# Kernel optimization log

Measured on AMD Instinct MI355X. Metric: run time of the kernel, lower is better.

Reference implementation:

```python
import jax, jax.numpy as jnp
import numpy as np

L = 4        # num_layers
N = 50000    # nodes
E = 500000   # edges
B = 32       # graphs
H = 64       # hidden_dim
HP = 16      # hidden_dim_pe
P = 8        # pe_dim
BN_EPS = 1e-5


def setup_inputs() -> dict:
    key = jax.random.key(0)
    ks = jax.random.split(key, 22)
    nrm = lambda k, s: jax.random.normal(k, s, dtype=jnp.float32)
    w = lambda k, s: nrm(k, s) * 0.1
    return {
        'x': nrm(ks[0], (N, H)),
        'pe': nrm(ks[1], (N, P)),
        'Lambda': jax.random.uniform(ks[2], (B, P), dtype=jnp.float32),
        'edge_attr': nrm(ks[3], (E, H)),
        'edge_index': jax.random.randint(ks[4], (2, E), 0, N),
        'batch': jnp.sort(jax.random.randint(ks[5], (N,), 0, B)),
        # edge encoder (SPE): eigenvalue MLP + output projection
        'We1': w(ks[6], (L, P, HP * P)), 'be1': jnp.zeros((L, HP * P)),
        'Wee': w(ks[7], (L, HP, H)),     'bee': jnp.zeros((L, H)),
        # GINE mlp: Linear-BN-ReLU-Linear
        'W1': w(ks[8], (L, H, H)), 'b1': jnp.zeros((L, H)),
        'g1': jnp.ones((L, H)),    'beta1': jnp.zeros((L, H)),
        'W2': w(ks[9], (L, H, H)), 'b2': jnp.zeros((L, H)),
        # equivariant PE conv: edge gate + channel Linear
        'Wg': w(ks[10], (L, H, HP)),  'bg': jnp.zeros((L, HP)),
        'Wp': w(ks[11], (L, HP, HP)), 'bp': jnp.zeros((L, HP)),
        # outer BatchNorm per layer
        'gn': jnp.ones((L, H)), 'bnb': jnp.zeros((L, H)),
    }


def _bn(h, gamma, beta):
    mu = h.mean(0)
    var = h.var(0)
    return gamma * (h - mu) * jax.lax.rsqrt(var + BN_EPS) + beta


def reference(x, pe, Lambda, edge_attr, We1, be1, Wee, bee, W1, b1, g1, beta1,
              W2, b2, Wg, bg, Wp, bp, gn, bnb, edge_index, batch):
    src, dst = edge_index[0], edge_index[1]
    bsrc = batch[src]                       # [E] graph id of source node
    z = jnp.tile(pe[:, None, :], (1, HP, 1))  # [N, HP, P]
    for i in range(L):
        # SPE edge encoder: phi(Lambda)-weighted inner product over pe axis
        phi = jax.nn.relu(Lambda @ We1[i] + be1[i]).reshape(B, HP, P)
        eh = jnp.einsum('ehp,ehp->eh', phi[bsrc] * z[src], z[dst])  # [E, HP]
        ea = eh @ Wee[i] + bee[i] + edge_attr                       # [E, H]
        # GINEConv: scatter-add of relu(x_src + edge_attr), eps = 0
        agg = jax.ops.segment_sum(jax.nn.relu(x[src] + ea), dst, num_segments=N)
        h = x + agg
        h = jax.nn.relu(_bn(h @ W1[i] + b1[i], g1[i], beta1[i])) @ W2[i] + b2[i]
        # GINConvEquivariant: gated scatter-add, Linear on channel axis
        gate = jax.nn.relu(ea @ Wg[i] + bg[i])                      # [E, HP]
        msgz = jax.nn.relu(z[src] + gate[:, :, None])               # [E, HP, P]
        z = z + jax.ops.segment_sum(msgz, dst, num_segments=N)
        z = jnp.einsum('nhp,hk->nkp', z, Wp[i]) + bp[i][None, :, None]
        x = _bn(h, gn[i], bnb[i])
        if i != L - 1:
            x = jax.nn.relu(x)
    return x, z
```

## Files before the change

### kernel.cpp

```cpp
#include <hip/hip_runtime.h>

#define NN 50000
#define EE 500000
#define LL 4

typedef unsigned short u16;
typedef unsigned int u32;

__device__ __forceinline__ float bfc(u16 u) { return __uint_as_float(((u32)u) << 16); }
__device__ __forceinline__ u16 f2bf(float f) {
    u32 u = __float_as_uint(f);
    return (u16)((u + 0x7fffu + ((u >> 16) & 1u)) >> 16);
}
__device__ __forceinline__ float lanebc(float v, int l) {
    return __int_as_float(__builtin_amdgcn_readlane(__float_as_int(v), l));
}
__device__ __forceinline__ void unpack2(u32 w, float& lo, float& hi) {
    lo = __uint_as_float(w << 16);
    hi = __uint_as_float(w & 0xffff0000u);
}

__global__ __launch_bounds__(256) void k_init(const float* __restrict__ x, float* __restrict__ Xf,
                                              u16* __restrict__ Xh, int big,
                                              int* __restrict__ deg, int* __restrict__ cursor,
                                              double* __restrict__ statsAll) {
    for (int i = blockIdx.x * 256 + threadIdx.x; i < NN * 64; i += gridDim.x * 256) {
        if (big) Xh[i] = f2bf(x[i]);
        else Xf[i] = x[i];
    }
    for (int i = blockIdx.x * 256 + threadIdx.x; i < NN; i += gridDim.x * 256) {
        deg[i] = 0;
        cursor[i] = 0;
    }
    for (int i = blockIdx.x * 256 + threadIdx.x; i < LL * 256; i += gridDim.x * 256)
        statsAll[i] = 0.0;
}

__global__ __launch_bounds__(128) void k_phi(const float* __restrict__ Lam, const float* __restrict__ We1,
                                             const float* __restrict__ be1, float* __restrict__ phiA) {
    int l = blockIdx.x >> 5, b = blockIdx.x & 31, j = threadIdx.x;
    float acc = be1[l * 128 + j];
    for (int q = 0; q < 8; q++)
        acc = fmaf(Lam[b * 8 + q], We1[l * 1024 + q * 128 + j], acc);
    phiA[l * 4096 + b * 128 + j] = fmaxf(acc, 0.f);
}

__global__ __launch_bounds__(256) void k_small(const float* __restrict__ Wee, const float* __restrict__ Wg,
                                               float* __restrict__ MA) {
    int l = blockIdx.x, t = threadIdx.x;
    int k = t >> 4, h = t & 15;
    float m = 0.f;
    for (int f = 0; f < 64; f++)
        m = fmaf(Wee[l * 1024 + k * 64 + f], Wg[l * 1024 + f * 16 + h], m);
    MA[l * 256 + t] = m;
}

__global__ __launch_bounds__(256) void k_hist(const int* __restrict__ ei, int* __restrict__ deg) {
    int e = blockIdx.x * 256 + threadIdx.x;
    if (e < EE) {
        int d = ei[EE + e];
        if (d >= 0 && d < NN) atomicAdd(&deg[d], 1);
    }
}

__global__ __launch_bounds__(256) void k_scan1(const int* __restrict__ deg, int* __restrict__ rowptr,
                                               int* __restrict__ bsum) {
    __shared__ int tmp[256];
    int t = threadIdx.x, i = blockIdx.x * 256 + t;
    int v = (i < NN) ? deg[i] : 0;
    tmp[t] = v;
    __syncthreads();
    for (int off = 1; off < 256; off <<= 1) {
        int a = (t >= off) ? tmp[t - off] : 0;
        __syncthreads();
        tmp[t] += a;
        __syncthreads();
    }
    if (i < NN) rowptr[i] = tmp[t] - v;
    if (t == 255) bsum[blockIdx.x] = tmp[255];
}

__global__ __launch_bounds__(256) void k_scan2(const int* __restrict__ bsum, int* __restrict__ boff,
                                               int* __restrict__ rowptr, int nb) {
    __shared__ int tmp[256];
    int t = threadIdx.x;
    int v = (t < nb) ? bsum[t] : 0;
    tmp[t] = v;
    __syncthreads();
    for (int off = 1; off < 256; off <<= 1) {
        int a = (t >= off) ? tmp[t - off] : 0;
        __syncthreads();
        tmp[t] += a;
        __syncthreads();
    }
    if (t < nb) boff[t] = tmp[t] - v;
    if (t == 255) rowptr[NN] = tmp[255];
}

__global__ __launch_bounds__(256) void k_scan3(int* __restrict__ rowptr, const int* __restrict__ boff) {
    int i = blockIdx.x * 256 + threadIdx.x;
    if (i < NN) rowptr[i] += boff[blockIdx.x];
}

__global__ __launch_bounds__(256) void k_scatter(const int* __restrict__ ei, const int* __restrict__ batch,
                                                 const int* __restrict__ rowptr, int* __restrict__ cursor,
                                                 u32* __restrict__ sb, int* __restrict__ eeo) {
    int e = blockIdx.x * 256 + threadIdx.x;
    if (e < EE) {
        int s = ei[e], d = ei[EE + e];
        if (s < 0) s = 0; if (s >= NN) s = NN - 1;
        if (d < 0) d = 0; if (d >= NN) d = NN - 1;
        int pos = rowptr[d] + atomicAdd(&cursor[d], 1);
        if (pos >= 0 && pos < EE) {
            sb[pos] = (u32)s | ((u32)(batch[s] & 31) << 16);
            eeo[pos] = e;
        }
    }
}

__global__ __launch_bounds__(256) void k_perm(const float* __restrict__ eat, const int* __restrict__ eeo,
                                              u16* __restrict__ eatp) {
    const float4* e4 = reinterpret_cast<const float4*>(eat);
    ushort4* o4 = reinterpret_cast<ushort4*>(eatp);
    for (long long i = (long long)blockIdx.x * 256 + threadIdx.x; i < (long long)EE * 16;
         i += (long long)gridDim.x * 256) {
        int idx = (int)(i >> 4), cc = (int)(i & 15);
        int e = eeo[idx];
        float4 v = e4[(size_t)e * 16 + cc];
        ushort4 o;
        o.x = f2bf(v.x); o.y = f2bf(v.y); o.z = f2bf(v.z); o.w = f2bf(v.w);
        o4[i] = o;
    }
}

__global__ __launch_bounds__(256) void k_eag_all(const u16* __restrict__ eatp, const float* __restrict__ Wg,
                                                 const float* __restrict__ bee, const float* __restrict__ bg,
                                                 u32* __restrict__ EAGp4) {
    __shared__ float sWg[4096];
    __shared__ float scv[64];
    __shared__ u32 srow[256][33];
    const int t = threadIdx.x;
    for (int i = t; i < 4096; i += 256) sWg[i] = Wg[i];
    __syncthreads();
    if (t < 64) {
        const int l = t >> 4, h = t & 15;
        float c = bg[l * 16 + h];
        for (int j = 0; j < 64; j++) c = fmaf(bee[l * 64 + j], sWg[l * 1024 + j * 16 + h], c);
        scv[t] = c;
    }
    const int base = blockIdx.x * 256;
    const u32* eat32 = (const u32*)eatp;
    for (int i = t; i < 256 * 32; i += 256) {
        int r = i >> 5, c = i & 31;
        int idx = base + r;
        srow[r][c] = (idx < EE) ? eat32[(size_t)idx * 32 + c] : 0u;
    }
    __syncthreads();
    const int idx = base + t;
    if (idx >= EE) return;
#pragma unroll
    for (int l = 0; l < LL; l++) {
        const float* wl = &sWg[l * 1024];
        float acc[16];
#pragma unroll
        for (int h = 0; h < 16; h++) acc[h] = scv[l * 16 + h];
#pragma unroll
        for (int c = 0; c < 32; c++) {
            float a0, a1;
            unpack2(srow[t][c], a0, a1);
            const float* w0 = &wl[(2 * c) * 16];
#pragma unroll
            for (int h = 0; h < 16; h++) acc[h] = fmaf(a0, w0[h], fmaf(a1, w0[16 + h], acc[h]));
        }
        u32 w[8];
#pragma unroll
        for (int h = 0; h < 8; h++) w[h] = (u32)f2bf(acc[h]) | ((u32)f2bf(acc[8 + h]) << 16);
        uint4* op = reinterpret_cast<uint4*>(EAGp4 + (size_t)l * EE * 8 + (size_t)idx * 8);
        op[0] = make_uint4(w[0], w[1], w[2], w[3]);
        op[1] = make_uint4(w[4], w[5], w[6], w[7]);
    }
}

__global__ __launch_bounds__(256) void k_eag2(const u16* __restrict__ eatp, const float* __restrict__ WgL,
                                              const float* __restrict__ beeL, const float* __restrict__ bgL,
                                              u32* __restrict__ EAGp) {
    __shared__ float sWg[1024];
    __shared__ float scv[16];
    __shared__ u32 srow[256][33];
    const int t = threadIdx.x;
    for (int i = t; i < 1024; i += 256) sWg[i] = WgL[i];
    __syncthreads();
    if (t < 16) {
        float c = bgL[t];
        for (int j = 0; j < 64; j++) c = fmaf(beeL[j], sWg[j * 16 + t], c);
        scv[t] = c;
    }
    const int base = blockIdx.x * 256;
    const u32* eat32 = (const u32*)eatp;
    for (int i = t; i < 256 * 32; i += 256) {
        int r = i >> 5, c = i & 31;
        int idx = base + r;
        srow[r][c] = (idx < EE) ? eat32[(size_t)idx * 32 + c] : 0u;
    }
    __syncthreads();
    const int idx = base + t;
    if (idx < EE) {
        float acc[16];
#pragma unroll
        for (int h = 0; h < 16; h++) acc[h] = scv[h];
#pragma unroll
        for (int c = 0; c < 32; c++) {
            float a0, a1;
            unpack2(srow[t][c], a0, a1);
            const float* w0 = &sWg[(2 * c) * 16];
#pragma unroll
            for (int h = 0; h < 16; h++) acc[h] = fmaf(a0, w0[h], fmaf(a1, w0[16 + h], acc[h]));
        }
        u32 w[8];
#pragma unroll
        for (int h = 0; h < 8; h++) w[h] = (u32)f2bf(acc[h]) | ((u32)f2bf(acc[8 + h]) << 16);
        uint4* op = reinterpret_cast<uint4*>(EAGp + (size_t)idx * 8);
        op[0] = make_uint4(w[0], w[1], w[2], w[3]);
        op[1] = make_uint4(w[4], w[5], w[6], w[7]);
    }
}

#define EF(P, kk) do { \
    P##w = (u32)__builtin_amdgcn_readlane((int)svec, (kk)); \
    int s_ = (int)(P##w & 0xffffu); \
    if (INM == 0) { P##z0 = P##z1 = pe[s_ * 8 + pp]; } \
    else { float2 t_ = Z2[s_ * 64 + lane]; P##z0 = t_.x; P##z1 = t_.y; } \
    P##xs = XBN ? fmaxf(0.f, fmaf(bfc(Xh[s_ * 64 + lane]), gmx, gax)) \
                : bfc(Xh[s_ * 64 + lane]); \
    size_t ge_ = (size_t)(c + (kk)); \
    P##ea = bfc(eatp[ge_ * 64 + lane]); \
    unpack2(EAGp[ge_ * 8 + hlo], P##gl, P##gh); \
} while (0)

#define EC(P, MSK) do { \
    int b_ = (int)((P##w >> 16) & 31u); \
    float p0 = sphi[b_ * 128 + lane] * P##z0 * zd0; \
    float p1 = sphi[b_ * 128 + 64 + lane] * P##z1 * zd1; \
    p0 += __shfl_xor(p0, 1); p1 += __shfl_xor(p1, 1); \
    p0 += __shfl_xor(p0, 2); p1 += __shfl_xor(p1, 2); \
    p0 += __shfl_xor(p0, 4); p1 += __shfl_xor(p1, 4); \
    float eaA = 0.f, eaB = 0.f, gA = P##gl, gB = 0.f, hA = P##gh, hB = 0.f; \
    _Pragma("unroll") \
    for (int k_ = 0; k_ < 8; k_++) { float e_ = lanebc(p0, k_ << 3); \
        eaA = fmaf(e_, wee[k_], eaA); gA = fmaf(e_, mlo[k_], gA); hA = fmaf(e_, mhi[k_], hA); } \
    _Pragma("unroll") \
    for (int k_ = 0; k_ < 8; k_++) { float e_ = lanebc(p1, k_ << 3); \
        eaB = fmaf(e_, wee[8 + k_], eaB); gB = fmaf(e_, mlo[8 + k_], gB); hB = fmaf(e_, mhi[8 + k_], hB); } \
    float ea_ = beev + P##ea + eaA + eaB; \
    accx = fmaf(MSK, fmaxf(0.f, P##xs + ea_), accx); \
    az0  = fmaf(MSK, fmaxf(0.f, P##z0 + fmaxf(gA + gB, 0.f)), az0); \
    az1  = fmaf(MSK, fmaxf(0.f, P##z1 + fmaxf(hA + hB, 0.f)), az1); \
} while (0)

template <int INM, int FIN, int XBN>
__global__ __launch_bounds__(256) void k_edge2(const float2* __restrict__ Z2,
                                               const float* __restrict__ pe,
                                               const u16* __restrict__ Xh,
                                               const u16* __restrict__ eatp, const u32* __restrict__ EAGp,
                                               const int* __restrict__ rowptr, const u32* __restrict__ sb,
                                               const float* __restrict__ phiL, const float* __restrict__ WeeL,
                                               const float* __restrict__ beeL, const float* __restrict__ ML,
                                               const float* __restrict__ WpL, const float* __restrict__ bpL,
                                               float* __restrict__ Hf, float2* __restrict__ Z2O,
                                               float* __restrict__ outz,
                                               const float* __restrict__ gnP, const float* __restrict__ bnbP,
                                               const double* __restrict__ s2P, const double* __restrict__ q2P) {
    __shared__ float sphi[4096];
    __shared__ float sWp[256];
    __shared__ float sbp[16];
    for (int t = threadIdx.x; t < 4096; t += 256) sphi[t] = phiL[t];
    if (threadIdx.x < 256) sWp[threadIdx.x] = WpL[threadIdx.x];
    if (threadIdx.x < 16) sbp[threadIdx.x] = bpL[threadIdx.x];
    const int lane = threadIdx.x & 63;
    const int wid = threadIdx.x >> 6;
    const int hlo = lane >> 3;
    const int pp = lane & 7;
    float wee[16], mlo[16], mhi[16];
#pragma unroll
    for (int k = 0; k < 16; k++) {
        wee[k] = WeeL[k * 64 + lane];
        mlo[k] = ML[k * 16 + hlo];
        mhi[k] = ML[k * 16 + 8 + hlo];
    }
    const float beev = beeL[lane];
    float gmx = 1.f, gax = 0.f;
    if (XBN) {
        const double mu = s2P[lane] * (1.0 / NN);
        const double var = q2P[lane] * (1.0 / NN) - mu * mu;
        const float inv = rsqrtf(fmaxf((float)var, 0.f) + 1e-5f);
        gmx = gnP[lane] * inv;
        gax = bnbP[lane] - (float)mu * gmx;
    }
    __syncthreads();
    for (int n = blockIdx.x * 4 + wid; n < NN; n += gridDim.x * 4) {
        float zd0, zd1;
        if (INM == 0) { zd0 = zd1 = pe[n * 8 + pp]; }
        else { float2 t = Z2[n * 64 + lane]; zd0 = t.x; zd1 = t.y; }
        float accx = XBN ? fmaxf(0.f, fmaf(bfc(Xh[n * 64 + lane]), gmx, gax))
                         : bfc(Xh[n * 64 + lane]);
        float az0 = zd0, az1 = zd1;
        int i0 = rowptr[n], i1 = rowptr[n + 1];
        if (i0 < 0) i0 = 0;
        if (i1 > EE) i1 = EE;
        for (int c = i0; c < i1; c += 64) {
            const int ce = (c + 64 < i1) ? c + 64 : i1;
            const int m = ce - c;
            const int mL = m - 1;
            int ci = c + lane; if (ci > i1 - 1) ci = i1 - 1;
            const u32 svec = sb[ci];
            u32 Aw, Bw, Nw, Mw;
            float Az0, Az1, Axs, Aea, Agl, Agh;
            float Bz0, Bz1, Bxs, Bea, Bgl, Bgh;
            float Nz0, Nz1, Nxs, Nea, Ngl, Ngh;
            float Mz0, Mz1, Mxs, Mea, Mgl, Mgh;
            EF(A, 0);
            EF(B, (1 > mL ? mL : 1));
            for (int k = 0; k < m; k += 2) {
                const int n0 = (k + 2 > mL) ? mL : k + 2;
                const int n1 = (k + 3 > mL) ? mL : k + 3;
                EF(N, n0);
                EF(M, n1);
                EC(A, 1.f);
                EC(B, (k + 1 <= mL) ? 1.f : 0.f);
                Aw = Nw; Az0 = Nz0; Az1 = Nz1; Axs = Nxs; Aea = Nea; Agl = Ngl; Agh = Ngh;
                Bw = Mw; Bz0 = Mz0; Bz1 = Mz1; Bxs = Mxs; Bea = Mea; Bgl = Mgl; Bgh = Mgh;
            }
        }
        Hf[n * 64 + lane] = accx;
        float r0 = sbp[hlo], r1 = sbp[8 + hlo];
#pragma unroll
        for (int h = 0; h < 8; h++) {
            const float v = __shfl(az0, (h << 3) + pp);
            r0 = fmaf(v, sWp[h * 16 + hlo], r0);
            r1 = fmaf(v, sWp[h * 16 + 8 + hlo], r1);
        }
#pragma unroll
        for (int h = 0; h < 8; h++) {
            const float v = __shfl(az1, (h << 3) + pp);
            r0 = fmaf(v, sWp[(8 + h) * 16 + hlo], r0);
            r1 = fmaf(v, sWp[(8 + h) * 16 + 8 + hlo], r1);
        }
        if (FIN) {
            outz[n * 128 + lane] = r0;
            outz[n * 128 + 64 + lane] = r1;
        } else {
            Z2O[n * 64 + lane] = make_float2(r0, r1);
        }
    }
}

template <int INM>
__global__ __launch_bounds__(256) void k_edge_s(const float* __restrict__ Zf,
                                                const float* __restrict__ pe,
                                                const float* __restrict__ Xf, const float* __restrict__ eat,
                                                const int* __restrict__ rowptr, const u32* __restrict__ sb,
                                                const int* __restrict__ eeo,
                                                const float* __restrict__ phiL, const float* __restrict__ WeeL,
                                                const float* __restrict__ beeL,
                                                const float* __restrict__ WgL, const float* __restrict__ bgL,
                                                const float* __restrict__ WpL, const float* __restrict__ bpL,
                                                float* __restrict__ Hf, float* __restrict__ ZfO,
                                                double* __restrict__ stats) {
    __shared__ float sphi[32 * 128];
    __shared__ float sWp[256];
    __shared__ float sbp[16];
    if (blockIdx.x == 0) stats[threadIdx.x] = 0.0;
    for (int t = threadIdx.x; t < 4096; t += 256) sphi[t] = phiL[t];
    if (threadIdx.x < 256) sWp[threadIdx.x] = WpL[threadIdx.x];
    if (threadIdx.x < 16) sbp[threadIdx.x] = bpL[threadIdx.x];
    const int lane = threadIdx.x & 63;
    const int wid = threadIdx.x >> 6;
    const int hlo = lane >> 3;
    const int pp = lane & 7;
    const int h16 = lane & 15;
    const int g16 = lane & 48;
    float wee[16], wgr[16];
#pragma unroll
    for (int k = 0; k < 16; k++) {
        wee[k] = WeeL[k * 64 + lane];
        wgr[k] = WgL[(g16 + k) * 16 + h16];
    }
    const float beev = beeL[lane];
    const float bgr = bgL[h16];
    __syncthreads();
    for (int n = blockIdx.x * 4 + wid; n < NN; n += gridDim.x * 4) {
        float zd0, zd1;
        if (INM == 0) { zd0 = zd1 = pe[n * 8 + pp]; }
        else { zd0 = Zf[n * 128 + lane]; zd1 = Zf[n * 128 + 64 + lane]; }
        float accx = Xf[n * 64 + lane];
        float az0 = zd0, az1 = zd1;
        int i0 = rowptr[n], i1 = rowptr[n + 1];
        if (i0 < 0) i0 = 0;
        if (i1 > EE) i1 = EE;
        for (int idx = i0; idx < i1; ++idx) {
            const u32 w = sb[idx];
            const int s = w & 0xffff;
            const int b = (w >> 16) & 31;
            int e = eeo[idx];
            e = (e < 0) ? 0 : ((e >= EE) ? EE - 1 : e);
            float zs0, zs1;
            if (INM == 0) { zs0 = zs1 = pe[s * 8 + pp]; }
            else { zs0 = Zf[s * 128 + lane]; zs1 = Zf[s * 128 + 64 + lane]; }
            float p0 = sphi[b * 128 + lane] * zs0 * zd0;
            float p1 = sphi[b * 128 + 64 + lane] * zs1 * zd1;
            p0 += __shfl_xor(p0, 1); p1 += __shfl_xor(p1, 1);
            p0 += __shfl_xor(p0, 2); p1 += __shfl_xor(p1, 2);
            p0 += __shfl_xor(p0, 4); p1 += __shfl_xor(p1, 4);
            float ea = beev + eat[(size_t)e * 64 + lane];
#pragma unroll
            for (int k = 0; k < 8; k++) ea = fmaf(lanebc(p0, k << 3), wee[k], ea);
#pragma unroll
            for (int k = 0; k < 8; k++) ea = fmaf(lanebc(p1, k << 3), wee[8 + k], ea);
            float gp = 0.f;
#pragma unroll
            for (int i = 0; i < 16; i++) gp = fmaf(__shfl(ea, g16 + i), wgr[i], gp);
            gp += __shfl_xor(gp, 16);
            gp += __shfl_xor(gp, 32);
            const float gv = fmaxf(gp + bgr, 0.f);
            const float glo = __shfl(gv, hlo);
            const float ghi = __shfl(gv, 8 + hlo);
            const float xs = Xf[s * 64 + lane];
            accx += fmaxf(0.f, xs + ea);
            az0 += fmaxf(0.f, zs0 + glo);
            az1 += fmaxf(0.f, zs1 + ghi);
        }
        Hf[n * 64 + lane] = accx;
        float r0 = sbp[hlo], r1 = sbp[8 + hlo];
#pragma unroll
        for (int h = 0; h < 8; h++) {
            const float v = __shfl(az0, (h << 3) + pp);
            r0 = fmaf(v, sWp[h * 16 + hlo], r0);
            r1 = fmaf(v, sWp[h * 16 + 8 + hlo], r1);
        }
#pragma unroll
        for (int h = 0; h < 8; h++) {
            const float v = __shfl(az1, (h << 3) + pp);
            r0 = fmaf(v, sWp[(8 + h) * 16 + hlo], r0);
            r1 = fmaf(v, sWp[(8 + h) * 16 + 8 + hlo], r1);
        }
        ZfO[n * 128 + lane] = r0;
        ZfO[n * 128 + 64 + lane] = r1;
    }
}

__global__ __launch_bounds__(256) void k_gemm1(float* Buf, const float* __restrict__ WL,
                                               const float* __restrict__ bL,
                                               double* __restrict__ sum, double* __restrict__ sq) {
    __shared__ float sW[4096];
    __shared__ double red[512];
    for (int t = threadIdx.x; t < 4096; t += 256) sW[t] = WL[t];
    const int lane = threadIdx.x & 63, wid = threadIdx.x >> 6;
    const float bv = bL[lane];
    __syncthreads();
    double s = 0.0, q = 0.0;
    for (int n = blockIdx.x * 4 + wid; n < NN; n += gridDim.x * 4) {
        const float h = Buf[n * 64 + lane];
        float a0 = bv, a1 = 0.f;
#pragma unroll
        for (int k = 0; k < 32; k++) a0 = fmaf(lanebc(h, k), sW[k * 64 + lane], a0);
#pragma unroll
        for (int k = 32; k < 64; k++) a1 = fmaf(lanebc(h, k), sW[k * 64 + lane], a1);
        const float acc = a0 + a1;
        Buf[n * 64 + lane] = acc;
        s += (double)acc;
        q += (double)acc * (double)acc;
    }
    red[threadIdx.x] = s;
    red[256 + threadIdx.x] = q;
    __syncthreads();
    if (threadIdx.x < 64) {
        s = red[threadIdx.x] + red[threadIdx.x + 64] + red[threadIdx.x + 128] + red[threadIdx.x + 192];
        q = red[256 + threadIdx.x] + red[320 + threadIdx.x] + red[384 + threadIdx.x] + red[448 + threadIdx.x];
        atomicAdd(&sum[lane], s);
        atomicAdd(&sq[lane], q);
    }
}

__global__ __launch_bounds__(256) void k_gemm2(float* Buf, const float* __restrict__ WL,
                                               const float* __restrict__ bL,
                                               const float* __restrict__ gL, const float* __restrict__ betaL,
                                               const double* __restrict__ s1, const double* __restrict__ q1,
                                               double* __restrict__ sum, double* __restrict__ sq,
                                               int out16, u16* __restrict__ XhOut) {
    __shared__ float sW[4096];
    __shared__ double red[512];
    for (int t = threadIdx.x; t < 4096; t += 256) sW[t] = WL[t];
    const int lane = threadIdx.x & 63, wid = threadIdx.x >> 6;
    const float bv = bL[lane];
    const double mu = s1[lane] * (1.0 / NN);
    const double var = q1[lane] * (1.0 / NN) - mu * mu;
    const float inv = rsqrtf(fmaxf((float)var, 0.f) + 1e-5f);
    const float gm = gL[lane] * inv;
    const float ga = betaL[lane] - (float)mu * gm;
    __syncthreads();
    double s = 0.0, q = 0.0;
    for (int n = blockIdx.x * 4 + wid; n < NN; n += gridDim.x * 4) {
        const float v = Buf[n * 64 + lane];
        const float r = fmaxf(fmaf(v, gm, ga), 0.f);
        float a0 = bv, a1 = 0.f;
#pragma unroll
        for (int k = 0; k < 32; k++) a0 = fmaf(lanebc(r, k), sW[k * 64 + lane], a0);
#pragma unroll
        for (int k = 32; k < 64; k++) a1 = fmaf(lanebc(r, k), sW[k * 64 + lane], a1);
        const float acc = a0 + a1;
        if (out16) XhOut[n * 64 + lane] = f2bf(acc);
        else Buf[n * 64 + lane] = acc;
        s += (double)acc;
        q += (double)acc * (double)acc;
    }
    red[threadIdx.x] = s;
    red[256 + threadIdx.x] = q;
    __syncthreads();
    if (threadIdx.x < 64) {
        s = red[threadIdx.x] + red[threadIdx.x + 64] + red[threadIdx.x + 128] + red[threadIdx.x + 192];
        q = red[256 + threadIdx.x] + red[320 + threadIdx.x] + red[384 + threadIdx.x] + red[448 + threadIdx.x];
        atomicAdd(&sum[lane], s);
        atomicAdd(&sq[lane], q);
    }
}

__global__ __launch_bounds__(256) void k_bnout(const float* __restrict__ In, float* __restrict__ Xf,
                                               const double* __restrict__ s2, const double* __restrict__ q2,
                                               const float* __restrict__ gL, const float* __restrict__ bL,
                                               int dorelu) {
    int i = blockIdx.x * 256 + threadIdx.x;
    const int f = i & 63;
    const double mu = s2[f] * (1.0 / NN);
    const double var = q2[f] * (1.0 / NN) - mu * mu;
    const float inv = rsqrtf(fmaxf((float)var, 0.f) + 1e-5f);
    const float gm = gL[f] * inv;
    const float ga = bL[f] - (float)mu * gm;
    for (; i < NN * 64; i += gridDim.x * 256) {
        float o = fmaf(In[i], gm, ga);
        if (dorelu) o = fmaxf(o, 0.f);
        Xf[i] = o;
    }
}

extern "C" void kernel_launch(void* const* d_in, const int* in_sizes, int n_in,
                              void* d_out, int out_size, void* d_ws, size_t ws_size,
                              hipStream_t stream) {
    (void)in_sizes; (void)n_in; (void)out_size;
    const float* x    = (const float*)d_in[0];
    const float* pe   = (const float*)d_in[1];
    const float* Lam  = (const float*)d_in[2];
    const float* eat  = (const float*)d_in[3];
    const int*   ei   = (const int*)d_in[4];
    const int*   batch= (const int*)d_in[5];
    const float* We1  = (const float*)d_in[6];
    const float* be1  = (const float*)d_in[7];
    const float* Wee  = (const float*)d_in[8];
    const float* bee  = (const float*)d_in[9];
    const float* W1   = (const float*)d_in[10];
    const float* b1   = (const float*)d_in[11];
    const float* g1   = (const float*)d_in[12];
    const float* bt1  = (const float*)d_in[13];
    const float* W2   = (const float*)d_in[14];
    const float* b2   = (const float*)d_in[15];
    const float* Wg   = (const float*)d_in[16];
    const float* bg   = (const float*)d_in[17];
    const float* Wp   = (const float*)d_in[18];
    const float* bp   = (const float*)d_in[19];
    const float* gn   = (const float*)d_in[20];
    const float* bnb  = (const float*)d_in[21];

    float* Xf   = (float*)d_out;
    u16*   Xh   = (u16*)d_out;
    float* B    = (float*)d_out + 3200000;

    float* A    = (float*)d_ws;
    float* Hf   = A + 6400000;
    float* MA   = Hf + 3200000;
    float* phiA = MA + 1024;
    double* stats = (double*)(phiA + 16384);
    int* rowptr = (int*)(stats + LL * 256);
    int* deg    = rowptr + NN + 1;
    int* bsum   = deg + NN;
    int* boff   = bsum + 256;
    int* cursor = boff + 256;
    u32* sb     = (u32*)(cursor + NN);
    int* eeo    = (int*)(sb + EE);
    u16* eatp   = (u16*)(eeo + EE);
    u32* EAGp   = (u32*)(eatp + (size_t)EE * 64);
    const size_t NEED_BIG  = (size_t)((char*)(EAGp + (size_t)EE * 8) - (char*)d_ws);
    const size_t NEED_BIG2 = (size_t)((char*)(EAGp + (size_t)EE * 32) - (char*)d_ws);
    const bool big2 = (ws_size >= NEED_BIG2);
    const bool big  = (ws_size >= NEED_BIG);

    float2* A2 = (float2*)A;
    float2* B2 = (float2*)B;

    const int NB_N = (NN + 255) / 256;
    const int NB_E = (EE + 255) / 256;

    k_init<<<1024, 256, 0, stream>>>(x, Xf, Xh, big ? 1 : 0, deg, cursor, stats);
    k_phi<<<LL * 32, 128, 0, stream>>>(Lam, We1, be1, phiA);
    k_hist<<<NB_E, 256, 0, stream>>>(ei, deg);
    k_scan1<<<NB_N, 256, 0, stream>>>(deg, rowptr, bsum);
    k_scan2<<<1, 256, 0, stream>>>(bsum, boff, rowptr, NB_N);
    k_scan3<<<NB_N, 256, 0, stream>>>(rowptr, boff);
    k_scatter<<<NB_E, 256, 0, stream>>>(ei, batch, rowptr, cursor, sb, eeo);
    if (big) {
        k_small<<<LL, 256, 0, stream>>>(Wee, Wg, MA);
        k_perm<<<4096, 256, 0, stream>>>(eat, eeo, eatp);
        if (big2)
            k_eag_all<<<NB_E, 256, 0, stream>>>(eatp, Wg, bee, bg, EAGp);
    }

    for (int l = 0; l < LL; l++) {
        const float* WeeL = Wee + l * 1024;
        const float* beeL = bee + l * 64;
        const float* WgL  = Wg + l * 1024;
        const float* bgL  = bg + l * 16;
        const float* WpL  = Wp + l * 256;
        const float* bpL  = bp + l * 16;
        const float* phiL = phiA + l * 4096;
        const float* ML   = MA + l * 256;
        double* sl = stats + l * 256;
        if (big) {
            const u32* EAGl = big2 ? (EAGp + (size_t)l * EE * 8) : EAGp;
            if (!big2)
                k_eag2<<<NB_E, 256, 0, stream>>>(eatp, WgL, beeL, bgL, EAGp);
            const double* s2p = stats + (l - 1) * 256 + 128;
            const double* q2p = stats + (l - 1) * 256 + 192;
            const float* gnp  = gn + (l - 1) * 64;
            const float* bnbp = bnb + (l - 1) * 64;
            if (l == 0)
                k_edge2<0, 0, 0><<<6272, 256, 0, stream>>>(A2, pe, Xh, eatp, EAGl, rowptr, sb,
                                                           phiL, WeeL, beeL, ML, WpL, bpL,
                                                           Hf, A2, nullptr,
                                                           nullptr, nullptr, nullptr, nullptr);
            else if (l == 1)
                k_edge2<1, 0, 1><<<6272, 256, 0, stream>>>(A2, pe, Xh, eatp, EAGl, rowptr, sb,
                                                           phiL, WeeL, beeL, ML, WpL, bpL,
                                                           Hf, B2, nullptr,
                                                           gnp, bnbp, s2p, q2p);
            else if (l == 2)
                k_edge2<1, 0, 1><<<6272, 256, 0, stream>>>(B2, pe, Xh, eatp, EAGl, rowptr, sb,
                                                           phiL, WeeL, beeL, ML, WpL, bpL,
                                                           Hf, A2, nullptr,
                                                           gnp, bnbp, s2p, q2p);
            else
                k_edge2<1, 1, 1><<<6272, 256, 0, stream>>>(A2, pe, Xh, eatp, EAGl, rowptr, sb,
                                                           phiL, WeeL, beeL, ML, WpL, bpL,
                                                           Hf, nullptr, B,
                                                           gnp, bnbp, s2p, q2p);
            k_gemm1<<<512, 256, 0, stream>>>(Hf, W1 + l * 4096, b1 + l * 64, sl, sl + 64);
            k_gemm2<<<512, 256, 0, stream>>>(Hf, W2 + l * 4096, b2 + l * 64,
                                             g1 + l * 64, bt1 + l * 64, sl, sl + 64,
                                             sl + 128, sl + 192,
                                             (l < LL - 1) ? 1 : 0, Xh);
        } else {
            const float* Zin  = (l == 2) ? B : A;
            float*       Zout = (l == 1 || l == 3) ? B : A;
            if (l == 0)
                k_edge_s<0><<<2048, 256, 0, stream>>>(nullptr, pe, Xf, eat, rowptr, sb, eeo,
                                                      phiL, WeeL, beeL, WgL, bgL, WpL, bpL,
                                                      Hf, Zout, sl);
            else
                k_edge_s<1><<<2048, 256, 0, stream>>>(Zin, pe, Xf, eat, rowptr, sb, eeo,
                                                      phiL, WeeL, beeL, WgL, bgL, WpL, bpL,
                                                      Hf, Zout, sl);
            k_gemm1<<<512, 256, 0, stream>>>(Hf, W1 + l * 4096, b1 + l * 64, sl, sl + 64);
            k_gemm2<<<512, 256, 0, stream>>>(Hf, W2 + l * 4096, b2 + l * 64,
                                             g1 + l * 64, bt1 + l * 64, sl, sl + 64,
                                             sl + 128, sl + 192, 0, nullptr);
            k_bnout<<<1024, 256, 0, stream>>>(Hf, Xf, sl + 128, sl + 192,
                                              gn + l * 64, bnb + l * 64,
                                              (l == LL - 1) ? 0 : 1);
        }
    }
    if (big) {
        double* sl3 = stats + (LL - 1) * 256;
        k_bnout<<<1024, 256, 0, stream>>>(Hf, Xf, sl3 + 128, sl3 + 192,
                                          gn + (LL - 1) * 64, bnb + (LL - 1) * 64, 0);
    }
}
```

Baseline: 1.004 ms.

## Split each node's edge range across two waves with shared-memory reduction

The fused edge kernel previously had one wavefront walk a node's whole CSR edge range in a grid-stride loop. Now each block handles two nodes, and two wavefronts split each node's edge list in half. Their partial accumulators are combined through shared memory before the channel projection and store. This adds parallelism and shortens per-wave latency chains, but each block now reloads the 16KB phi table and weights for only two nodes, launches 25000 blocks, and adds a block-wide barrier.

Result: slower. 1.195 ms (+19.0%).

```diff
diff --git a/kernel.cpp b/kernel.cpp
--- a/kernel.cpp
+++ b/kernel.cpp
@@ -258,7 +258,7 @@
 } while (0)
 
 template <int INM, int FIN, int XBN>
-__global__ __launch_bounds__(256) void k_edge2(const float2* __restrict__ Z2,
+__global__ __launch_bounds__(256) void k_edge5(const float2* __restrict__ Z2,
                                                const float* __restrict__ pe,
                                                const u16* __restrict__ Xh,
                                                const u16* __restrict__ eatp, const u32* __restrict__ EAGp,
@@ -273,11 +273,14 @@
     __shared__ float sphi[4096];
     __shared__ float sWp[256];
     __shared__ float sbp[16];
+    __shared__ float sred[2][3][64];
     for (int t = threadIdx.x; t < 4096; t += 256) sphi[t] = phiL[t];
     if (threadIdx.x < 256) sWp[threadIdx.x] = WpL[threadIdx.x];
     if (threadIdx.x < 16) sbp[threadIdx.x] = bpL[threadIdx.x];
     const int lane = threadIdx.x & 63;
     const int wid = threadIdx.x >> 6;
+    const int g = wid >> 1;
+    const int half = wid & 1;
     const int hlo = lane >> 3;
     const int pp = lane & 7;
     float wee[16], mlo[16], mhi[16];
@@ -297,60 +300,78 @@
         gax = bnbP[lane] - (float)mu * gmx;
     }
     __syncthreads();
-    for (int n = blockIdx.x * 4 + wid; n < NN; n += gridDim.x * 4) {
-        float zd0, zd1;
-        if (INM == 0) { zd0 = zd1 = pe[n * 8 + pp]; }
-        else { float2 t = Z2[n * 64 + lane]; zd0 = t.x; zd1 = t.y; }
-        float accx = XBN ? fmaxf(0.f, fmaf(bfc(Xh[n * 64 + lane]), gmx, gax))
-                         : bfc(Xh[n * 64 + lane]);
-        float az0 = zd0, az1 = zd1;
-        int i0 = rowptr[n], i1 = rowptr[n + 1];
-        if (i0 < 0) i0 = 0;
-        if (i1 > EE) i1 = EE;
-        for (int c = i0; c < i1; c += 64) {
-            const int ce = (c + 64 < i1) ? c + 64 : i1;
-            const int m = ce - c;
-            const int mL = m - 1;
-            int ci = c + lane; if (ci > i1 - 1) ci = i1 - 1;
-            const u32 svec = sb[ci];
-            u32 Aw, Bw, Nw, Mw;
-            float Az0, Az1, Axs, Aea, Agl, Agh;
-            float Bz0, Bz1, Bxs, Bea, Bgl, Bgh;
-            float Nz0, Nz1, Nxs, Nea, Ngl, Ngh;
-            float Mz0, Mz1, Mxs, Mea, Mgl, Mgh;
-            EF(A, 0);
-            EF(B, (1 > mL ? mL : 1));
-            for (int k = 0; k < m; k += 2) {
-                const int n0 = (k + 2 > mL) ? mL : k + 2;
-                const int n1 = (k + 3 > mL) ? mL : k + 3;
-                EF(N, n0);
-                EF(M, n1);
-                EC(A, 1.f);
-                EC(B, (k + 1 <= mL) ? 1.f : 0.f);
-                Aw = Nw; Az0 = Nz0; Az1 = Nz1; Axs = Nxs; Aea = Nea; Agl = Ngl; Agh = Ngh;
-                Bw = Mw; Bz0 = Mz0; Bz1 = Mz1; Bxs = Mxs; Bea = Mea; Bgl = Mgl; Bgh = Mgh;
-            }
+
+    const int n = blockIdx.x * 2 + g;
+    float zd0, zd1;
+    if (INM == 0) { zd0 = zd1 = pe[n * 8 + pp]; }
+    else { float2 t = Z2[n * 64 + lane]; zd0 = t.x; zd1 = t.y; }
+    float accx, az0, az1;
+    if (half == 0) {
+        accx = XBN ? fmaxf(0.f, fmaf(bfc(Xh[n * 64 + lane]), gmx, gax))
+                   : bfc(Xh[n * 64 + lane]);
+        az0 = zd0; az1 = zd1;
+    } else {
+        accx = 0.f; az0 = 0.f; az1 = 0.f;
+    }
+    int i0 = rowptr[n], i1 = rowptr[n + 1];
+    if (i0 < 0) i0 = 0;
+    if (i1 > EE) i1 = EE;
+    const int mid = (i0 + i1 + 1) >> 1;
+    const int ws = half ? mid : i0;
+    const int we = half ? i1 : mid;
+    for (int c = ws; c < we; c += 64) {
+        const int ce = (c + 64 < we) ? c + 64 : we;
+        const int m = ce - c;
+        const int mL = m - 1;
+        int ci = c + lane; if (ci > we - 1) ci = we - 1;
+        const u32 svec = sb[ci];
+        u32 Aw, Bw, Nw, Mw;
+        float Az0, Az1, Axs, Aea, Agl, Agh;
+        float Bz0, Bz1, Bxs, Bea, Bgl, Bgh;
+        float Nz0, Nz1, Nxs, Nea, Ngl, Ngh;
+        float Mz0, Mz1, Mxs, Mea, Mgl, Mgh;
+        EF(A, 0);
+        EF(B, (1 > mL ? mL : 1));
+        for (int k = 0; k < m; k += 2) {
+            const int n0 = (k + 2 > mL) ? mL : k + 2;
+            const int n1 = (k + 3 > mL) ? mL : k + 3;
+            EF(N, n0);
+            EF(M, n1);
+            EC(A, 1.f);
+            EC(B, (k + 1 <= mL) ? 1.f : 0.f);
+            Aw = Nw; Az0 = Nz0; Az1 = Nz1; Axs = Nxs; Aea = Nea; Agl = Ngl; Agh = Ngh;
+            Bw = Mw; Bz0 = Mz0; Bz1 = Mz1; Bxs = Mxs; Bea = Mea; Bgl = Mgl; Bgh = Mgh;
         }
-        Hf[n * 64 + lane] = accx;
-        float r0 = sbp[hlo], r1 = sbp[8 + hlo];
-#pragma unroll
-        for (int h = 0; h < 8; h++) {
-            const float v = __shfl(az0, (h << 3) + pp);
-            r0 = fmaf(v, sWp[h * 16 + hlo], r0);
-            r1 = fmaf(v, sWp[h * 16 + 8 + hlo], r1);
-        }
-#pragma unroll
-        for (int h = 0; h < 8; h++) {
-            const float v = __shfl(az1, (h << 3) + pp);
-            r0 = fmaf(v, sWp[(8 + h) * 16 + hlo], r0);
-            r1 = fmaf(v, sWp[(8 + h) * 16 + 8 + hlo], r1);
-        }
-        if (FIN) {
-            outz[n * 128 + lane] = r0;
-            outz[n * 128 + 64 + lane] = r1;
-        } else {
-            Z2O[n * 64 + lane] = make_float2(r0, r1);
-        }
+    }
+    if (half == 1) {
+        sred[g][0][lane] = accx;
+        sred[g][1][lane] = az0;
+        sred[g][2][lane] = az1;
+    }
+    __syncthreads();
+    if (half == 1) return;
+    accx += sred[g][0][lane];
+    az0 += sred[g][1][lane];
+    az1 += sred[g][2][lane];
+    Hf[n * 64 + lane] = accx;
+    float r0 = sbp[hlo], r1 = sbp[8 + hlo];
+#pragma unroll
+    for (int h = 0; h < 8; h++) {
+        const float v = __shfl(az0, (h << 3) + pp);
+        r0 = fmaf(v, sWp[h * 16 + hlo], r0);
+        r1 = fmaf(v, sWp[h * 16 + 8 + hlo], r1);
+    }
+#pragma unroll
+    for (int h = 0; h < 8; h++) {
+        const float v = __shfl(az1, (h << 3) + pp);
+        r0 = fmaf(v, sWp[(8 + h) * 16 + hlo], r0);
+        r1 = fmaf(v, sWp[(8 + h) * 16 + 8 + hlo], r1);
+    }
+    if (FIN) {
+        outz[n * 128 + lane] = r0;
+        outz[n * 128 + 64 + lane] = r1;
+    } else {
+        Z2O[n * 64 + lane] = make_float2(r0, r1);
     }
 }
 
@@ -612,6 +633,8 @@
             k_eag_all<<<NB_E, 256, 0, stream>>>(eatp, Wg, bee, bg, EAGp);
     }
 
+    const int GE = NN / 2;
+
     for (int l = 0; l < LL; l++) {
         const float* WeeL = Wee + l * 1024;
         const float* beeL = bee + l * 64;
@@ -631,25 +654,25 @@
             const float* gnp  = gn + (l - 1) * 64;
             const float* bnbp = bnb + (l - 1) * 64;
             if (l == 0)
-                k_edge2<0, 0, 0><<<6272, 256, 0, stream>>>(A2, pe, Xh, eatp, EAGl, rowptr, sb,
-                                                           phiL, WeeL, beeL, ML, WpL, bpL,
-                                                           Hf, A2, nullptr,
-                                                           nullptr, nullptr, nullptr, nullptr);
+                k_edge5<0, 0, 0><<<GE, 256, 0, stream>>>(A2, pe, Xh, eatp, EAGl, rowptr, sb,
+                                                         phiL, WeeL, beeL, ML, WpL, bpL,
+                                                         Hf, A2, nullptr,
+                                                         nullptr, nullptr, nullptr, nullptr);
             else if (l == 1)
-                k_edge2<1, 0, 1><<<6272, 256, 0, stream>>>(A2, pe, Xh, eatp, EAGl, rowptr, sb,
-                                                           phiL, WeeL, beeL, ML, WpL, bpL,
-                                                           Hf, B2, nullptr,
-                                                           gnp, bnbp, s2p, q2p);
+                k_edge5<1, 0, 1><<<GE, 256, 0, stream>>>(A2, pe, Xh, eatp, EAGl, rowptr, sb,
+                                                         phiL, WeeL, beeL, ML, WpL, bpL,
+                                                         Hf, B2, nullptr,
+                                                         gnp, bnbp, s2p, q2p);
             else if (l == 2)
-                k_edge2<1, 0, 1><<<6272, 256, 0, stream>>>(B2, pe, Xh, eatp, EAGl, rowptr, sb,
-                                                           phiL, WeeL, beeL, ML, WpL, bpL,
-                                                           Hf, A2, nullptr,
-                                                           gnp, bnbp, s2p, q2p);
+                k_edge5<1, 0, 1><<<GE, 256, 0, stream>>>(B2, pe, Xh, eatp, EAGl, rowptr, sb,
+                                                         phiL, WeeL, beeL, ML, WpL, bpL,
+                                                         Hf, A2, nullptr,
+                                                         gnp, bnbp, s2p, q2p);
             else
-                k_edge2<1, 1, 1><<<6272, 256, 0, stream>>>(A2, pe, Xh, eatp, EAGl, rowptr, sb,
-                                                           phiL, WeeL, beeL, ML, WpL, bpL,
-                                                           Hf, nullptr, B,
-                                                           gnp, bnbp, s2p, q2p);
+                k_edge5<1, 1, 1><<<GE, 256, 0, stream>>>(A2, pe, Xh, eatp, EAGl, rowptr, sb,
+                                                         phiL, WeeL, beeL, ML, WpL, bpL,
+                                                         Hf, nullptr, B,
+                                                         gnp, bnbp, s2p, q2p);
             k_gemm1<<<512, 256, 0, stream>>>(Hf, W1 + l * 4096, b1 + l * 64, sl, sl + 64);
             k_gemm2<<<512, 256, 0, stream>>>(Hf, W2 + l * 4096, b2 + l * 64,
                                              g1 + l * 64, bt1 + l * 64, sl, sl + 64,
```
